# Kernel optimization log

Measured on AMD Instinct MI355X. Metric: run time of the kernel, lower is better.

## Reference

```python
import jax, jax.numpy as jnp
import numpy as np

N, E = 10000, 320000
IN, H, C, ED = 256, 4, 64, 64
HC = H * C
EPS = 1e-5
NEG_SLOPE = 0.2


def setup_inputs() -> dict:
    key = jax.random.key(0)
    ks = jax.random.split(key, 12)
    g = lambda k, shape, fan: jax.random.normal(k, shape, jnp.float32) * (1.0 / np.sqrt(fan))
    return {
        "x": jax.random.normal(ks[0], (N, IN), jnp.float32),
        "edge_index": jax.random.randint(ks[1], (2, E), 0, N, jnp.int64),
        "edge_attr": jax.random.normal(ks[2], (E, ED), jnp.float32),
        "Wl": g(ks[3], (HC, IN), IN),   # lin_l weight (source)
        "bl": jnp.zeros((HC,), jnp.float32),
        "Wr": g(ks[4], (HC, IN), IN),   # lin_r weight (target)
        "br": jnp.zeros((HC,), jnp.float32),
        "We": g(ks[5], (HC, ED), ED),   # lin_edge weight (no bias)
        "att": g(ks[6], (H, C), C),
        "bias": jnp.zeros((HC,), jnp.float32),
        "gamma": jnp.ones((HC,), jnp.float32),
        "beta": jnp.zeros((HC,), jnp.float32),
    }


def reference(x, edge_index, edge_attr, Wl, bl, Wr, br, We, att, bias, gamma, beta):
    src, dst = edge_index[0], edge_index[1]
    # add_self_loops with fill_value='mean': loop edge_attr = mean of incoming attrs
    ones = jnp.ones((E,), jnp.float32)
    cnt = jax.ops.segment_sum(ones, dst, num_segments=N)              # [N]
    loop_attr = jax.ops.segment_sum(edge_attr, dst, num_segments=N) / jnp.maximum(cnt, 1.0)[:, None]
    node_ids = jnp.arange(N, dtype=src.dtype)
    src_f = jnp.concatenate([src, node_ids])                          # [E+N]
    dst_f = jnp.concatenate([dst, node_ids])
    ea = jnp.concatenate([edge_attr, loop_attr], axis=0)              # [E+N, ED]

    xl = (x @ Wl.T + bl).reshape(N, H, C)   # source-side projection
    xr = (x @ Wr.T + br).reshape(N, H, C)   # target-side projection
    ep = (ea @ We.T).reshape(-1, H, C)       # edge projection

    m = xl[src_f] + xr[dst_f] + ep                                    # [E+N, H, C]
    m = jnp.where(m >= 0, m, NEG_SLOPE * m)                           # leaky_relu(0.2)
    logits = jnp.einsum("ehc,hc->eh", m, att)                        # [E+N, H]

    # segment softmax over target node dst_f (every node has a self loop)
    mx = jax.ops.segment_max(logits, dst_f, num_segments=N)
    ex = jnp.exp(logits - mx[dst_f])
    den = jax.ops.segment_sum(ex, dst_f, num_segments=N)
    alpha = ex / den[dst_f]                                           # [E+N, H]

    out = jax.ops.segment_sum(xl[src_f] * alpha[:, :, None], dst_f, num_segments=N)
    h = out.reshape(N, HC) + bias

    # SiLU then LayerNorm, dropout is identity in eval
    h = h * jax.nn.sigmoid(h)
    mu = jnp.mean(h, axis=-1, keepdims=True)
    var = jnp.mean((h - mu) ** 2, axis=-1, keepdims=True)
    h = (h - mu) * jax.lax.rsqrt(var + EPS) * gamma + beta
    return h, alpha
```

## Files before the change

### kernel.cpp

```cpp
#include <hip/hip_runtime.h>

#define N_NODES 10000
#define N_EDGES 320000
#define NE_TOT  330000
#define NEG_SLOPE 0.2f
#define LN_EPS 1e-5f

#define OFF_CNT    0u
#define OFF_FILL   40000u
#define OFF_ROWPTR 80128u
#define OFF_EIDS   120320u
#define OFF_POSE   1440512u
#define OFF_XLH    4000512u
#define OFF_XRH    9120512u
#define OFF_LOG    14240512u
#define OFF_WLF    19520512u
#define OFF_WRF    19651584u
#define OFF_WEF    19782656u
#define OFF_SD     19815424u
#define OFF_EAC    21135424u


typedef __bf16 bf16x8 __attribute__((ext_vector_type(8)));
typedef float  f32x4  __attribute__((ext_vector_type(4)));
typedef unsigned short us4 __attribute__((ext_vector_type(4)));

__device__ __forceinline__ float bf2f(unsigned short u) {
    union { unsigned int i; float f; } v;
    v.i = ((unsigned int)u) << 16;
    return v.f;
}
__device__ __forceinline__ float lo2f(unsigned int u) {
    union { unsigned int i; float f; } v;
    v.i = u << 16;
    return v.f;
}
__device__ __forceinline__ float hi2f(unsigned int u) {
    union { unsigned int i; float f; } v;
    v.i = u & 0xFFFF0000u;
    return v.f;
}
__device__ __forceinline__ unsigned short f2bf(float x) {
    __bf16 b = (__bf16)x;
    return __builtin_bit_cast(unsigned short, b);
}
__device__ __forceinline__ bf16x8 cvt8(const float* p) {
    float4 v0 = *reinterpret_cast<const float4*>(p);
    float4 v1 = *reinterpret_cast<const float4*>(p + 4);
    bf16x8 t;
    t[0] = (__bf16)v0.x; t[1] = (__bf16)v0.y; t[2] = (__bf16)v0.z; t[3] = (__bf16)v0.w;
    t[4] = (__bf16)v1.x; t[5] = (__bf16)v1.y; t[6] = (__bf16)v1.z; t[7] = (__bf16)v1.w;
    return t;
}

__global__ void k_pre(const int* __restrict__ ei, int* __restrict__ cnt,
                      const float* __restrict__ Wl, const float* __restrict__ Wr,
                      const float* __restrict__ We,
                      unsigned short* __restrict__ wlf,
                      unsigned short* __restrict__ wrf,
                      unsigned short* __restrict__ wef) {
    int gid = blockIdx.x * 256 + threadIdx.x;
    if (gid < 8192) {
        int idx = gid;
        int ln = idx & 63;
        int ts = (idx >> 6) & 7;
        int ct = idx >> 9;
        int c = ct * 16 + (ln & 15);
        int k0 = ts * 32 + (ln >> 4) * 8;
        *reinterpret_cast<bf16x8*>(wlf + (size_t)idx * 8) = cvt8(Wl + (size_t)c * 256 + k0);
        *reinterpret_cast<bf16x8*>(wrf + (size_t)idx * 8) = cvt8(Wr + (size_t)c * 256 + k0);
        if (idx < 2048) {
            int f = idx >> 6;
            int cb = f >> 1, step = f & 1;
            int ce = cb * 16 + (ln & 15);
            int ke = step * 32 + (ln >> 4) * 8;
            *reinterpret_cast<bf16x8*>(wef + (size_t)idx * 8) = cvt8(We + (size_t)ce * 64 + ke);
        }
    } else {
        int e = gid - 8192;
        if (e < N_EDGES) atomicAdd(&cnt[ei[N_EDGES + e]], 1);
    }
}

__global__ void k_scan(const int* __restrict__ cnt, int* __restrict__ row_ptr) {
    __shared__ int sums[1024];
    int t = threadIdx.x;
    const int CH = 10;
    int base = t * CH;
    int s = 0;
    for (int i = 0; i < CH; i++) {
        int n = base + i;
        if (n < N_NODES) s += cnt[n] + 1;
    }
    sums[t] = s;
    __syncthreads();
    for (int off = 1; off < 1024; off <<= 1) {
        int v = (t >= off) ? sums[t - off] : 0;
        __syncthreads();
        sums[t] += v;
        __syncthreads();
    }
    int run = (t == 0) ? 0 : sums[t - 1];
    for (int i = 0; i < CH; i++) {
        int n = base + i;
        if (n < N_NODES) { row_ptr[n] = run; run += cnt[n] + 1; }
    }
    if (t == 1023) row_ptr[N_NODES] = sums[1023];
}

__global__ void k_fill(const int* __restrict__ ei, const int* __restrict__ row_ptr,
                       int* __restrict__ fill, int* __restrict__ eids,
                       int* __restrict__ sdv, int* __restrict__ pose) {
    int e = blockIdx.x * blockDim.x + threadIdx.x;
    if (e >= NE_TOT) return;
    int s, d;
    if (e < N_EDGES) { s = ei[e]; d = ei[N_EDGES + e]; }
    else             { s = e - N_EDGES; d = s; }
    int pos = atomicAdd(&fill[d], 1);
    int p = row_ptr[d] + pos;
    eids[p] = e;
    sdv[p] = s | (d << 16);
    pose[e] = p;
}

__global__ void k_permute_e(const float* __restrict__ edge_attr,
                            const int* __restrict__ pose,
                            unsigned short* __restrict__ eac) {
    int idx = blockIdx.x * blockDim.x + threadIdx.x;
    if (idx >= N_EDGES * 32) return;
    int e = idx >> 5, cp = idx & 31;
    float2 v = reinterpret_cast<const float2*>(edge_attr)[(size_t)e * 32 + cp];
    int p = pose[e];
    unsigned int u = ((unsigned int)f2bf(v.x)) | (((unsigned int)f2bf(v.y)) << 16);
    reinterpret_cast<unsigned int*>(eac)[(size_t)p * 32 + cp] = u;
}

__global__ void k_self_attr(const int* __restrict__ row_ptr,
                            const int* __restrict__ pose,
                            unsigned short* __restrict__ eac) {
    int node = (blockIdx.x << 2) + (threadIdx.x >> 6);
    int lane = threadIdx.x & 63;
    int b = row_ptr[node], en = row_ptr[node + 1];
    int selfp = pose[N_EDGES + node];
    float s0 = 0.0f, s1 = 0.0f;
    int i = b;
    for (; i + 1 < en; i += 2) {
        float a0 = bf2f(eac[(size_t)(i + 0) * 64 + lane]);
        float a1 = bf2f(eac[(size_t)(i + 1) * 64 + lane]);
        s0 += (i + 0 == selfp) ? 0.0f : a0;
        s1 += (i + 1 == selfp) ? 0.0f : a1;
    }
    for (; i < en; i++) {
        float a = bf2f(eac[(size_t)i * 64 + lane]);
        s0 += (i == selfp) ? 0.0f : a;
    }
    float s = s0 + s1;
    float c = (float)(en - b - 1);
    eac[(size_t)selfp * 64 + lane] = f2bf(s / fmaxf(c, 1.0f));
}

__global__ __launch_bounds__(256) void k_gemm_mfma(
        const float* __restrict__ x,
        const float* __restrict__ bl, const float* __restrict__ br,
        const unsigned short* __restrict__ wlf,
        const unsigned short* __restrict__ wrf,
        unsigned short* __restrict__ xlh,
        unsigned short* __restrict__ xrh) {
    __shared__ __bf16 xs[8 * 64 * 8];
    int tid = threadIdx.x;
    int nb = blockIdx.x * 16;

    for (int f = tid; f < 512; f += 256) {
        int t = f >> 6, ln = f & 63;
        int node = nb + (ln & 15);
        int k0 = t * 32 + (ln >> 4) * 8;
        *reinterpret_cast<bf16x8*>(&xs[f * 8]) = cvt8(x + (size_t)node * 256 + k0);
    }
    __syncthreads();

    int lane = tid & 63;
    int wv = tid >> 6;
    int quad = lane >> 4;
    int ln15 = lane & 15;

    bf16x8 bfr[8];
#pragma unroll
    for (int t = 0; t < 8; t++)
        bfr[t] = *reinterpret_cast<const bf16x8*>(&xs[(t * 64 + lane) * 8]);

    int node = nb + ln15;
#pragma unroll
    for (int ci = 0; ci < 4; ci++) {
        int ct = wv * 4 + ci;
        f32x4 accl, accr;
        accl[0] = accl[1] = accl[2] = accl[3] = 0.0f;
        accr[0] = accr[1] = accr[2] = accr[3] = 0.0f;
#pragma unroll
        for (int t = 0; t < 8; t++) {
            bf16x8 al = *reinterpret_cast<const bf16x8*>(
                wlf + ((size_t)(ct * 8 + t) * 64 + lane) * 8);
            accl = __builtin_amdgcn_mfma_f32_16x16x32_bf16(al, bfr[t], accl, 0, 0, 0);
        }
#pragma unroll
        for (int t = 0; t < 8; t++) {
            bf16x8 ar = *reinterpret_cast<const bf16x8*>(
                wrf + ((size_t)(ct * 8 + t) * 64 + lane) * 8);
            accr = __builtin_amdgcn_mfma_f32_16x16x32_bf16(ar, bfr[t], accr, 0, 0, 0);
        }
        int cbase = ct * 16 + quad * 4;
        int fidx  = quad * 64 + ct * 4;
        float4 blv = *reinterpret_cast<const float4*>(bl + cbase);
        float4 brv = *reinterpret_cast<const float4*>(br + cbase);
        us4 ol, orr;
        ol[0] = f2bf(accl[0] + blv.x); ol[1] = f2bf(accl[1] + blv.y);
        ol[2] = f2bf(accl[2] + blv.z); ol[3] = f2bf(accl[3] + blv.w);
        orr[0] = f2bf(accr[0] + brv.x); orr[1] = f2bf(accr[1] + brv.y);
        orr[2] = f2bf(accr[2] + brv.z); orr[3] = f2bf(accr[3] + brv.w);
        *reinterpret_cast<us4*>(xlh + (size_t)node * 256 + fidx) = ol;
        *reinterpret_cast<us4*>(xrh + (size_t)node * 256 + fidx) = orr;
    }
}

__global__ __launch_bounds__(256) void k_logits_v4(
        const int* __restrict__ sdv,
        const unsigned short* __restrict__ eac,
        const unsigned short* __restrict__ xlh,
        const unsigned short* __restrict__ xrh,
        const unsigned short* __restrict__ wef,
        const float* __restrict__ att,
        float* __restrict__ logits) {
    __shared__ __bf16 wef_s[2048 * 8];
    __shared__ float att_s[256];
    int tid = threadIdx.x;

    for (int f = tid; f < 2048; f += 256) {
        *reinterpret_cast<bf16x8*>(&wef_s[(size_t)f * 8]) =
            *reinterpret_cast<const bf16x8*>(wef + (size_t)f * 8);
    }
    if (tid < 64) {
        reinterpret_cast<float4*>(att_s)[tid] =
            reinterpret_cast<const float4*>(att)[tid];
    }
    __syncthreads();

    int lane = tid & 63;
    int wv = tid >> 6;
    int quad = lane >> 4;
    int ln15 = lane & 15;

    const int ntiles = NE_TOT / 16;
#pragma unroll 1
    for (int t = blockIdx.x * 4 + wv; t < ntiles; t += gridDim.x * 4) {
        int pos = t * 16 + ln15;
        int sd = sdv[pos];
        int s = sd & 0xFFFF;
        int d = sd >> 16;
        const unsigned short* row = eac + (size_t)pos * 64;
        const uint4* xls = reinterpret_cast<const uint4*>(
            xlh + (size_t)s * 256 + quad * 64);
        const uint4* xrd = reinterpret_cast<const uint4*>(
            xrh + (size_t)d * 256 + quad * 64);

        bf16x8 bfr0 = *reinterpret_cast<const bf16x8*>(row + quad * 8);
        bf16x8 bfr1 = *reinterpret_cast<const bf16x8*>(row + 32 + quad * 8);
        uint4 xa[8], xb[8];
#pragma unroll
        for (int k = 0; k < 8; k++) {
            xa[k] = xls[k];
            xb[k] = xrd[k];
        }
        __builtin_amdgcn_sched_barrier(0);

        float hsum[4] = {0.0f, 0.0f, 0.0f, 0.0f};
#pragma unroll
        for (int cb = 0; cb < 16; cb++) {
            f32x4 acc;
            acc[0] = acc[1] = acc[2] = acc[3] = 0.0f;
            bf16x8 a0 = *reinterpret_cast<const bf16x8*>(
                &wef_s[((size_t)(cb * 2 + 0) * 64 + lane) * 8]);
            bf16x8 a1 = *reinterpret_cast<const bf16x8*>(
                &wef_s[((size_t)(cb * 2 + 1) * 64 + lane) * 8]);
            acc = __builtin_amdgcn_mfma_f32_16x16x32_bf16(a0, bfr0, acc, 0, 0, 0);
            acc = __builtin_amdgcn_mfma_f32_16x16x32_bf16(a1, bfr1, acc, 0, 0, 0);

            unsigned int u0 = (cb & 1) ? xa[cb >> 1].z : xa[cb >> 1].x;
            unsigned int u1 = (cb & 1) ? xa[cb >> 1].w : xa[cb >> 1].y;
            unsigned int w0 = (cb & 1) ? xb[cb >> 1].z : xb[cb >> 1].x;
            unsigned int w1 = (cb & 1) ? xb[cb >> 1].w : xb[cb >> 1].y;

            int cbase = cb * 16 + quad * 4;
            float4 at = *reinterpret_cast<const float4*>(&att_s[cbase]);
            float v0 = acc[0] + lo2f(u0) + lo2f(w0); v0 = fmaxf(v0, NEG_SLOPE * v0);
            float v1 = acc[1] + hi2f(u0) + hi2f(w0); v1 = fmaxf(v1, NEG_SLOPE * v1);
            float v2 = acc[2] + lo2f(u1) + lo2f(w1); v2 = fmaxf(v2, NEG_SLOPE * v2);
            float v3 = acc[3] + hi2f(u1) + hi2f(w1); v3 = fmaxf(v3, NEG_SLOPE * v3);
            float hs = fmaf(v0, at.x, fmaf(v1, at.y, fmaf(v2, at.z, v3 * at.w)));
            hsum[cb >> 2] += hs;
        }
#pragma unroll
        for (int hh = 0; hh < 4; hh++) {
            hsum[hh] += __shfl_xor(hsum[hh], 16, 64);
            hsum[hh] += __shfl_xor(hsum[hh], 32, 64);
        }
        if (quad == 0) {
            reinterpret_cast<float4*>(logits)[pos] =
                make_float4(hsum[0], hsum[1], hsum[2], hsum[3]);
        }
    }
}

__global__ void k_aggregate(const int* __restrict__ sdv,
                            const int* __restrict__ row_ptr,
                            const int* __restrict__ eids,
                            const float* __restrict__ logits,
                            const unsigned short* __restrict__ xlh,
                            const float* __restrict__ bias,
                            const float* __restrict__ gamma,
                            const float* __restrict__ beta,
                            float* __restrict__ hout,
                            float* __restrict__ alpha_out) {
    int node = (blockIdx.x << 2) + (threadIdx.x >> 6);
    int lane = threadIdx.x & 63;
    int h = lane >> 4;
    int b = row_ptr[node], en = row_ptr[node + 1];
    const uint2* xl2 = reinterpret_cast<const uint2*>(xlh);
    int ci  = (lane & 3) * 16 + (lane >> 2);
    int cb4 = (lane >> 2) * 4 + (lane & 3);

    float m0 = -INFINITY, m1 = -INFINITY, m2 = -INFINITY, m3 = -INFINITY;
    int i = b;
    for (; i + 3 < en; i += 4) {
        m0 = fmaxf(m0, logits[(i + 0) * 4 + h]);
        m1 = fmaxf(m1, logits[(i + 1) * 4 + h]);
        m2 = fmaxf(m2, logits[(i + 2) * 4 + h]);
        m3 = fmaxf(m3, logits[(i + 3) * 4 + h]);
    }
    for (; i < en; i++) m0 = fmaxf(m0, logits[i * 4 + h]);
    float mh = fmaxf(fmaxf(m0, m1), fmaxf(m2, m3));

    float d0 = 0.0f, d1 = 0.0f, d2 = 0.0f, d3 = 0.0f;
    i = b;
    for (; i + 3 < en; i += 4) {
        d0 += __expf(logits[(i + 0) * 4 + h] - mh);
        d1 += __expf(logits[(i + 1) * 4 + h] - mh);
        d2 += __expf(logits[(i + 2) * 4 + h] - mh);
        d3 += __expf(logits[(i + 3) * 4 + h] - mh);
    }
    for (; i < en; i++) d0 += __expf(logits[i * 4 + h] - mh);
    float rden = 1.0f / ((d0 + d1) + (d2 + d3));

    float4 ac0; ac0.x = ac0.y = ac0.z = ac0.w = 0.0f;
    float4 ac1; ac1.x = ac1.y = ac1.z = ac1.w = 0.0f;
    i = b;
    for (; i + 7 < en; i += 8) {
        int sd0 = sdv[i + 0], sd1 = sdv[i + 1], sd2 = sdv[i + 2], sd3 = sdv[i + 3];
        int sd4 = sdv[i + 4], sd5 = sdv[i + 5], sd6 = sdv[i + 6], sd7 = sdv[i + 7];
        float lg0 = logits[(i + 0) * 4 + h], lg1 = logits[(i + 1) * 4 + h];
        float lg2 = logits[(i + 2) * 4 + h], lg3 = logits[(i + 3) * 4 + h];
        float lg4 = logits[(i + 4) * 4 + h], lg5 = logits[(i + 5) * 4 + h];
        float lg6 = logits[(i + 6) * 4 + h], lg7 = logits[(i + 7) * 4 + h];
        int e0 = eids[i + 0], e1 = eids[i + 1], e2 = eids[i + 2], e3 = eids[i + 3];
        int e4 = eids[i + 4], e5 = eids[i + 5], e6 = eids[i + 6], e7 = eids[i + 7];
        uint2 x0 = xl2[(size_t)(sd0 & 0xFFFF) * 64 + ci];
        uint2 x1 = xl2[(size_t)(sd1 & 0xFFFF) * 64 + ci];
        uint2 x2 = xl2[(size_t)(sd2 & 0xFFFF) * 64 + ci];
        uint2 x3 = xl2[(size_t)(sd3 & 0xFFFF) * 64 + ci];
        uint2 x4 = xl2[(size_t)(sd4 & 0xFFFF) * 64 + ci];
        uint2 x5 = xl2[(size_t)(sd5 & 0xFFFF) * 64 + ci];
        uint2 x6 = xl2[(size_t)(sd6 & 0xFFFF) * 64 + ci];
        uint2 x7 = xl2[(size_t)(sd7 & 0xFFFF) * 64 + ci];
        asm volatile("" : "+v"(x0.x), "+v"(x0.y), "+v"(x1.x), "+v"(x1.y),
                          "+v"(x2.x), "+v"(x2.y), "+v"(x3.x), "+v"(x3.y));
        asm volatile("" : "+v"(x4.x), "+v"(x4.y), "+v"(x5.x), "+v"(x5.y),
                          "+v"(x6.x), "+v"(x6.y), "+v"(x7.x), "+v"(x7.y));

        float al0 = __expf(lg0 - mh) * rden;
        float al1 = __expf(lg1 - mh) * rden;
        float al2 = __expf(lg2 - mh) * rden;
        float al3 = __expf(lg3 - mh) * rden;
        float al4 = __expf(lg4 - mh) * rden;
        float al5 = __expf(lg5 - mh) * rden;
        float al6 = __expf(lg6 - mh) * rden;
        float al7 = __expf(lg7 - mh) * rden;
        if ((lane & 15) == 0) {
            alpha_out[e0 * 4 + h] = al0; alpha_out[e1 * 4 + h] = al1;
            alpha_out[e2 * 4 + h] = al2; alpha_out[e3 * 4 + h] = al3;
            alpha_out[e4 * 4 + h] = al4; alpha_out[e5 * 4 + h] = al5;
            alpha_out[e6 * 4 + h] = al6; alpha_out[e7 * 4 + h] = al7;
        }
        ac0.x = fmaf(al0, lo2f(x0.x), ac0.x); ac0.y = fmaf(al0, hi2f(x0.x), ac0.y);
        ac0.z = fmaf(al0, lo2f(x0.y), ac0.z); ac0.w = fmaf(al0, hi2f(x0.y), ac0.w);
        ac1.x = fmaf(al1, lo2f(x1.x), ac1.x); ac1.y = fmaf(al1, hi2f(x1.x), ac1.y);
        ac1.z = fmaf(al1, lo2f(x1.y), ac1.z); ac1.w = fmaf(al1, hi2f(x1.y), ac1.w);
        ac0.x = fmaf(al2, lo2f(x2.x), ac0.x); ac0.y = fmaf(al2, hi2f(x2.x), ac0.y);
        ac0.z = fmaf(al2, lo2f(x2.y), ac0.z); ac0.w = fmaf(al2, hi2f(x2.y), ac0.w);
        ac1.x = fmaf(al3, lo2f(x3.x), ac1.x); ac1.y = fmaf(al3, hi2f(x3.x), ac1.y);
        ac1.z = fmaf(al3, lo2f(x3.y), ac1.z); ac1.w = fmaf(al3, hi2f(x3.y), ac1.w);
        ac0.x = fmaf(al4, lo2f(x4.x), ac0.x); ac0.y = fmaf(al4, hi2f(x4.x), ac0.y);
        ac0.z = fmaf(al4, lo2f(x4.y), ac0.z); ac0.w = fmaf(al4, hi2f(x4.y), ac0.w);
        ac1.x = fmaf(al5, lo2f(x5.x), ac1.x); ac1.y = fmaf(al5, hi2f(x5.x), ac1.y);
        ac1.z = fmaf(al5, lo2f(x5.y), ac1.z); ac1.w = fmaf(al5, hi2f(x5.y), ac1.w);
        ac0.x = fmaf(al6, lo2f(x6.x), ac0.x); ac0.y = fmaf(al6, hi2f(x6.x), ac0.y);
        ac0.z = fmaf(al6, lo2f(x6.y), ac0.z); ac0.w = fmaf(al6, hi2f(x6.y), ac0.w);
        ac1.x = fmaf(al7, lo2f(x7.x), ac1.x); ac1.y = fmaf(al7, hi2f(x7.x), ac1.y);
        ac1.z = fmaf(al7, lo2f(x7.y), ac1.z); ac1.w = fmaf(al7, hi2f(x7.y), ac1.w);
    }
    for (; i < en; i++) {
        int e = eids[i];
        int s = sdv[i] & 0xFFFF;
        float al = __expf(logits[i * 4 + h] - mh) * rden;
        if ((lane & 15) == 0) alpha_out[e * 4 + h] = al;
        uint2 xv = xl2[(size_t)s * 64 + ci];
        ac0.x = fmaf(al, lo2f(xv.x), ac0.x); ac0.y = fmaf(al, hi2f(xv.x), ac0.y);
        ac0.z = fmaf(al, lo2f(xv.y), ac0.z); ac0.w = fmaf(al, hi2f(xv.y), ac0.w);
    }
    float4 acc;
    acc.x = ac0.x + ac1.x;
    acc.y = ac0.y + ac1.y;
    acc.z = ac0.z + ac1.z;
    acc.w = ac0.w + ac1.w;

    const float4 b4 = reinterpret_cast<const float4*>(bias)[cb4];
    float4 hv;
    hv.x = acc.x + b4.x; hv.y = acc.y + b4.y;
    hv.z = acc.z + b4.z; hv.w = acc.w + b4.w;
    hv.x = hv.x / (1.0f + __expf(-hv.x));
    hv.y = hv.y / (1.0f + __expf(-hv.y));
    hv.z = hv.z / (1.0f + __expf(-hv.z));
    hv.w = hv.w / (1.0f + __expf(-hv.w));
    float s1 = hv.x + hv.y + hv.z + hv.w;
    float s2 = hv.x * hv.x + hv.y * hv.y + hv.z * hv.z + hv.w * hv.w;
#pragma unroll
    for (int off = 1; off < 64; off <<= 1) {
        s1 += __shfl_xor(s1, off, 64);
        s2 += __shfl_xor(s2, off, 64);
    }
    float mu = s1 * (1.0f / 256.0f);
    float var = s2 * (1.0f / 256.0f) - mu * mu;
    float rs = rsqrtf(var + LN_EPS);
    const float4 g4 = reinterpret_cast<const float4*>(gamma)[cb4];
    const float4 be4 = reinterpret_cast<const float4*>(beta)[cb4];
    float4 o;
    o.x = (hv.x - mu) * rs * g4.x + be4.x;
    o.y = (hv.y - mu) * rs * g4.y + be4.y;
    o.z = (hv.z - mu) * rs * g4.z + be4.z;
    o.w = (hv.w - mu) * rs * g4.w + be4.w;
    reinterpret_cast<float4*>(hout)[node * 64 + cb4] = o;
}

extern "C" void kernel_launch(void* const* d_in, const int* in_sizes, int n_in,
                              void* d_out, int out_size, void* d_ws, size_t ws_size,
                              hipStream_t stream) {
    (void)in_sizes; (void)n_in; (void)out_size; (void)ws_size;
    const float* x         = (const float*)d_in[0];
    const int*   ei        = (const int*)d_in[1];
    const float* edge_attr = (const float*)d_in[2];
    const float* Wl        = (const float*)d_in[3];
    const float* bl        = (const float*)d_in[4];
    const float* Wr        = (const float*)d_in[5];
    const float* br        = (const float*)d_in[6];
    const float* We        = (const float*)d_in[7];
    const float* att       = (const float*)d_in[8];
    const float* bias      = (const float*)d_in[9];
    const float* gamma     = (const float*)d_in[10];
    const float* beta      = (const float*)d_in[11];

    char* ws = (char*)d_ws;
    int*   cnt     = (int*)(ws + OFF_CNT);
    int*   fill    = (int*)(ws + OFF_FILL);
    int*   row_ptr = (int*)(ws + OFF_ROWPTR);
    int*   eids    = (int*)(ws + OFF_EIDS);
    int*   pose    = (int*)(ws + OFF_POSE);
    unsigned short* xlh = (unsigned short*)(ws + OFF_XLH);
    unsigned short* xrh = (unsigned short*)(ws + OFF_XRH);
    float* logits  = (float*)(ws + OFF_LOG);
    unsigned short* wlf = (unsigned short*)(ws + OFF_WLF);
    unsigned short* wrf = (unsigned short*)(ws + OFF_WRF);
    unsigned short* wef = (unsigned short*)(ws + OFF_WEF);
    int*   sdv     = (int*)(ws + OFF_SD);
    unsigned short* eac = (unsigned short*)(ws + OFF_EAC);

    float* hout      = (float*)d_out;
    float* alpha_out = (float*)d_out + N_NODES * 256;

    hipMemsetAsync(ws + OFF_CNT, 0, 2 * N_NODES * sizeof(int), stream);

    k_pre<<<(8192 + N_EDGES) / 256, 256, 0, stream>>>(ei, cnt, Wl, Wr, We,
                                                      wlf, wrf, wef);
    k_scan<<<1, 1024, 0, stream>>>(cnt, row_ptr);
    k_fill<<<(NE_TOT + 255) / 256, 256, 0, stream>>>(ei, row_ptr, fill, eids, sdv, pose);
    k_gemm_mfma<<<N_NODES / 16, 256, 0, stream>>>(x, bl, br, wlf, wrf, xlh, xrh);
    k_permute_e<<<(N_EDGES * 32) / 256, 256, 0, stream>>>(edge_attr, pose, eac);
    k_self_attr<<<N_NODES / 4, 256, 0, stream>>>(row_ptr, pose, eac);
    k_logits_v4<<<2048, 256, 0, stream>>>(sdv, eac, xlh, xrh, wef, att, logits);
    k_aggregate<<<N_NODES / 4, 256, 0, stream>>>(sdv, row_ptr, eids, logits, xlh,
                                                 bias, gamma, beta, hout, alpha_out);
}
```

Baseline: 358.2 us.

## Split each node's edge list across four waves in aggregate kernel

The aggregation kernel now assigns one node per 256-thread block instead of one node per wave. Each of the four waves handles a quarter of the incoming edges, and the partial max, denominator and accumulator are combined through shared memory with block barriers. This exposes more memory-level parallelism and shortens the per-wave serial gather chain, since there are about 33 edges per node. The cost is three barriers per block, more blocks to launch, and an LDS reduction, while only one wave does the final LayerNorm.

```diff
diff --git a/kernel.cpp b/kernel.cpp
--- a/kernel.cpp
+++ b/kernel.cpp
@@ -309,50 +309,64 @@
     }
 }
 
-__global__ void k_aggregate(const int* __restrict__ sdv,
-                            const int* __restrict__ row_ptr,
-                            const int* __restrict__ eids,
-                            const float* __restrict__ logits,
-                            const unsigned short* __restrict__ xlh,
-                            const float* __restrict__ bias,
-                            const float* __restrict__ gamma,
-                            const float* __restrict__ beta,
-                            float* __restrict__ hout,
-                            float* __restrict__ alpha_out) {
-    int node = (blockIdx.x << 2) + (threadIdx.x >> 6);
-    int lane = threadIdx.x & 63;
+__global__ __launch_bounds__(256) void k_aggregate(
+        const int* __restrict__ sdv,
+        const int* __restrict__ row_ptr,
+        const int* __restrict__ eids,
+        const float* __restrict__ logits,
+        const unsigned short* __restrict__ xlh,
+        const float* __restrict__ bias,
+        const float* __restrict__ gamma,
+        const float* __restrict__ beta,
+        float* __restrict__ hout,
+        float* __restrict__ alpha_out) {
+    __shared__ float lsm[16];
+    __shared__ float lsd[16];
+    __shared__ float4 acc_lds[256];
+    int tid = threadIdx.x;
+    int wv = tid >> 6, lane = tid & 63;
+    int node = blockIdx.x;
     int h = lane >> 4;
     int b = row_ptr[node], en = row_ptr[node + 1];
+    int len = en - b;
     const uint2* xl2 = reinterpret_cast<const uint2*>(xlh);
     int ci  = (lane & 3) * 16 + (lane >> 2);
     int cb4 = (lane >> 2) * 4 + (lane & 3);
 
-    float m0 = -INFINITY, m1 = -INFINITY, m2 = -INFINITY, m3 = -INFINITY;
-    int i = b;
-    for (; i + 3 < en; i += 4) {
+    int seg = (len + 3) >> 2;
+    int sb = b + wv * seg;
+    int se = sb + seg; if (se > en) se = en;
+    if (sb > en) sb = en;
+
+    float m0 = -INFINITY, m1 = -INFINITY;
+    int i = sb;
+    for (; i + 1 < se; i += 2) {
         m0 = fmaxf(m0, logits[(i + 0) * 4 + h]);
         m1 = fmaxf(m1, logits[(i + 1) * 4 + h]);
-        m2 = fmaxf(m2, logits[(i + 2) * 4 + h]);
-        m3 = fmaxf(m3, logits[(i + 3) * 4 + h]);
-    }
-    for (; i < en; i++) m0 = fmaxf(m0, logits[i * 4 + h]);
-    float mh = fmaxf(fmaxf(m0, m1), fmaxf(m2, m3));
-
-    float d0 = 0.0f, d1 = 0.0f, d2 = 0.0f, d3 = 0.0f;
-    i = b;
-    for (; i + 3 < en; i += 4) {
+    }
+    for (; i < se; i++) m0 = fmaxf(m0, logits[i * 4 + h]);
+    float mseg = fmaxf(m0, m1);
+    if ((lane & 15) == 0) lsm[wv * 4 + h] = mseg;
+    __syncthreads();
+    float mh = fmaxf(fmaxf(lsm[0 * 4 + h], lsm[1 * 4 + h]),
+                     fmaxf(lsm[2 * 4 + h], lsm[3 * 4 + h]));
+
+    float d0 = 0.0f, d1 = 0.0f;
+    i = sb;
+    for (; i + 1 < se; i += 2) {
         d0 += __expf(logits[(i + 0) * 4 + h] - mh);
         d1 += __expf(logits[(i + 1) * 4 + h] - mh);
-        d2 += __expf(logits[(i + 2) * 4 + h] - mh);
-        d3 += __expf(logits[(i + 3) * 4 + h] - mh);
-    }
-    for (; i < en; i++) d0 += __expf(logits[i * 4 + h] - mh);
-    float rden = 1.0f / ((d0 + d1) + (d2 + d3));
+    }
+    for (; i < se; i++) d0 += __expf(logits[i * 4 + h] - mh);
+    if ((lane & 15) == 0) lsd[wv * 4 + h] = d0 + d1;
+    __syncthreads();
+    float rden = 1.0f / ((lsd[0 * 4 + h] + lsd[1 * 4 + h]) +
+                         (lsd[2 * 4 + h] + lsd[3 * 4 + h]));
 
     float4 ac0; ac0.x = ac0.y = ac0.z = ac0.w = 0.0f;
     float4 ac1; ac1.x = ac1.y = ac1.z = ac1.w = 0.0f;
-    i = b;
-    for (; i + 7 < en; i += 8) {
+    i = sb;
+    for (; i + 7 < se; i += 8) {
         int sd0 = sdv[i + 0], sd1 = sdv[i + 1], sd2 = sdv[i + 2], sd3 = sdv[i + 3];
         int sd4 = sdv[i + 4], sd5 = sdv[i + 5], sd6 = sdv[i + 6], sd7 = sdv[i + 7];
         float lg0 = logits[(i + 0) * 4 + h], lg1 = logits[(i + 1) * 4 + h];
@@ -405,7 +419,7 @@
         ac1.x = fmaf(al7, lo2f(x7.x), ac1.x); ac1.y = fmaf(al7, hi2f(x7.x), ac1.y);
         ac1.z = fmaf(al7, lo2f(x7.y), ac1.z); ac1.w = fmaf(al7, hi2f(x7.y), ac1.w);
     }
-    for (; i < en; i++) {
+    for (; i < se; i++) {
         int e = eids[i];
         int s = sdv[i] & 0xFFFF;
         float al = __expf(logits[i * 4 + h] - mh) * rden;
@@ -414,38 +428,52 @@
         ac0.x = fmaf(al, lo2f(xv.x), ac0.x); ac0.y = fmaf(al, hi2f(xv.x), ac0.y);
         ac0.z = fmaf(al, lo2f(xv.y), ac0.z); ac0.w = fmaf(al, hi2f(xv.y), ac0.w);
     }
-    float4 acc;
-    acc.x = ac0.x + ac1.x;
-    acc.y = ac0.y + ac1.y;
-    acc.z = ac0.z + ac1.z;
-    acc.w = ac0.w + ac1.w;
-
-    const float4 b4 = reinterpret_cast<const float4*>(bias)[cb4];
-    float4 hv;
-    hv.x = acc.x + b4.x; hv.y = acc.y + b4.y;
-    hv.z = acc.z + b4.z; hv.w = acc.w + b4.w;
-    hv.x = hv.x / (1.0f + __expf(-hv.x));
-    hv.y = hv.y / (1.0f + __expf(-hv.y));
-    hv.z = hv.z / (1.0f + __expf(-hv.z));
-    hv.w = hv.w / (1.0f + __expf(-hv.w));
-    float s1 = hv.x + hv.y + hv.z + hv.w;
-    float s2 = hv.x * hv.x + hv.y * hv.y + hv.z * hv.z + hv.w * hv.w;
-#pragma unroll
-    for (int off = 1; off < 64; off <<= 1) {
-        s1 += __shfl_xor(s1, off, 64);
-        s2 += __shfl_xor(s2, off, 64);
-    }
-    float mu = s1 * (1.0f / 256.0f);
-    float var = s2 * (1.0f / 256.0f) - mu * mu;
-    float rs = rsqrtf(var + LN_EPS);
-    const float4 g4 = reinterpret_cast<const float4*>(gamma)[cb4];
-    const float4 be4 = reinterpret_cast<const float4*>(beta)[cb4];
-    float4 o;
-    o.x = (hv.x - mu) * rs * g4.x + be4.x;
-    o.y = (hv.y - mu) * rs * g4.y + be4.y;
-    o.z = (hv.z - mu) * rs * g4.z + be4.z;
-    o.w = (hv.w - mu) * rs * g4.w + be4.w;
-    reinterpret_cast<float4*>(hout)[node * 64 + cb4] = o;
+    float4 accp;
+    accp.x = ac0.x + ac1.x;
+    accp.y = ac0.y + ac1.y;
+    accp.z = ac0.z + ac1.z;
+    accp.w = ac0.w + ac1.w;
+    acc_lds[tid] = accp;
+    __syncthreads();
+
+    if (tid < 64) {
+        float4 a0 = acc_lds[tid];
+        float4 a1 = acc_lds[tid + 64];
+        float4 a2 = acc_lds[tid + 128];
+        float4 a3 = acc_lds[tid + 192];
+        float4 acc;
+        acc.x = (a0.x + a1.x) + (a2.x + a3.x);
+        acc.y = (a0.y + a1.y) + (a2.y + a3.y);
+        acc.z = (a0.z + a1.z) + (a2.z + a3.z);
+        acc.w = (a0.w + a1.w) + (a2.w + a3.w);
+
+        const float4 b4 = reinterpret_cast<const float4*>(bias)[cb4];
+        float4 hv;
+        hv.x = acc.x + b4.x; hv.y = acc.y + b4.y;
+        hv.z = acc.z + b4.z; hv.w = acc.w + b4.w;
+        hv.x = hv.x / (1.0f + __expf(-hv.x));
+        hv.y = hv.y / (1.0f + __expf(-hv.y));
+        hv.z = hv.z / (1.0f + __expf(-hv.z));
+        hv.w = hv.w / (1.0f + __expf(-hv.w));
+        float s1 = hv.x + hv.y + hv.z + hv.w;
+        float s2 = hv.x * hv.x + hv.y * hv.y + hv.z * hv.z + hv.w * hv.w;
+#pragma unroll
+        for (int off = 1; off < 64; off <<= 1) {
+            s1 += __shfl_xor(s1, off, 64);
+            s2 += __shfl_xor(s2, off, 64);
+        }
+        float mu = s1 * (1.0f / 256.0f);
+        float var = s2 * (1.0f / 256.0f) - mu * mu;
+        float rs = rsqrtf(var + LN_EPS);
+        const float4 g4 = reinterpret_cast<const float4*>(gamma)[cb4];
+        const float4 be4 = reinterpret_cast<const float4*>(beta)[cb4];
+        float4 o;
+        o.x = (hv.x - mu) * rs * g4.x + be4.x;
+        o.y = (hv.y - mu) * rs * g4.y + be4.y;
+        o.z = (hv.z - mu) * rs * g4.z + be4.z;
+        o.w = (hv.w - mu) * rs * g4.w + be4.w;
+        reinterpret_cast<float4*>(hout)[node * 64 + cb4] = o;
+    }
 }
 
 extern "C" void kernel_launch(void* const* d_in, const int* in_sizes, int n_in,
@@ -493,6 +521,6 @@
     k_permute_e<<<(N_EDGES * 32) / 256, 256, 0, stream>>>(edge_attr, pose, eac);
     k_self_attr<<<N_NODES / 4, 256, 0, stream>>>(row_ptr, pose, eac);
     k_logits_v4<<<2048, 256, 0, stream>>>(sdv, eac, xlh, xrh, wef, att, logits);
-    k_aggregate<<<N_NODES / 4, 256, 0, stream>>>(sdv, row_ptr, eids, logits, xlh,
-                                                 bias, gamma, beta, hout, alpha_out);
-}
+    k_aggregate<<<N_NODES, 256, 0, stream>>>(sdv, row_ptr, eids, logits, xlh,
+                                             bias, gamma, beta, hout, alpha_out);
+}
```

Measured after the change: 365.0 us. No clear change (+1.9%).
